# Performance work log

Measured on AMD Instinct MI355X. Metric: run time of the kernel, lower is better.

Reference implementation:

```python
import jax, jax.numpy as jnp
import numpy as np

D_HEAD = 64

def setup_inputs() -> dict:
    key = jax.random.key(0)
    ks = jax.random.split(key, 5)
    B, N, d_feat, d = 8, 2048, 256, 3
    f = jax.random.normal(ks[0], (B, N, d_feat), dtype=jnp.float32)
    x_tilde = jax.random.normal(ks[1], (B, N, d), dtype=jnp.float32)
    log_eps = jax.random.normal(ks[2], (B,), dtype=jnp.float32)
    W_q = jax.random.normal(ks[3], (d_feat + 1, D_HEAD), dtype=jnp.float32) * (1.0 / np.sqrt(d_feat + 1))
    W_k = jax.random.normal(ks[4], (d_feat + 1, D_HEAD), dtype=jnp.float32) * (1.0 / np.sqrt(d_feat + 1))
    return {"f": f, "x_tilde": x_tilde, "log_eps": log_eps, "W_q": W_q, "W_k": W_k}

def reference(f, x_tilde, log_eps, W_q, W_k):
    B, N, _ = f.shape
    # concat per-cloud log_eps scalar to every particle's features
    le = jnp.broadcast_to(log_eps[:, None, None], (B, N, 1)).astype(f.dtype)
    fc = jnp.concatenate([f, le], axis=-1)            # (B, N, d_feat+1)
    q = jnp.einsum('bnf,fh->bnh', fc, W_q)            # (B, N, d_head)
    k = jnp.einsum('bnf,fh->bnh', fc, W_k)            # (B, N, d_head)
    scale = jnp.asarray(np.sqrt(float(D_HEAD)), dtype=f.dtype)
    logits = jnp.einsum('bnh,bmh->bnm', q, k) / scale  # (B, N, N)
    N_f = jnp.asarray(N, dtype=f.dtype)
    col_softmax = jax.nn.softmax(logits, axis=1)       # softmax over QUERY axis
    pi = col_softmax / N_f                             # (B, N, N)
    # y_tilde = N * pi^T @ x_tilde
    y_tilde = N_f * jnp.einsum('bnm,bnd->bmd', pi, x_tilde)  # (B, N, d)
    return y_tilde, pi
```

## Files before the change

kernel.cpp:

```cpp
#include <hip/hip_runtime.h>
#include <hip/hip_bf16.h>

#define BB 8
#define NN 2048
#define DF 256
#define HH 64

using bf16x8 = __attribute__((ext_vector_type(8))) short;
using f32x4  = __attribute__((ext_vector_type(4))) float;
typedef unsigned short u16;

__global__ __launch_bounds__(256) void qk_proj_kernel(
    const float* __restrict__ f, const float* __restrict__ log_eps,
    const float* __restrict__ Wq, const float* __restrict__ Wk,
    __hip_bfloat16* __restrict__ Qs, __hip_bfloat16* __restrict__ Ks)
{
    __shared__ float wql[64 * 64];
    __shared__ float wkl[64 * 64];
    const int tid = threadIdx.x;
    const int h  = tid & 63;
    const int rg = tid >> 6;
    const int row_base = blockIdx.x * 32;
    const int b = row_base >> 11;

    const float le = log_eps[b];
    const float wq_last = Wq[DF * HH + h];
    const float wk_last = Wk[DF * HH + h];
    float q[8], k[8];
#pragma unroll
    for (int j = 0; j < 8; ++j) { q[j] = le * wq_last; k[j] = le * wk_last; }

    for (int kc = 0; kc < 4; ++kc) {
        __syncthreads();
#pragma unroll
        for (int it = 0; it < 4; ++it) {
            int idx = (tid + it * 256) * 4;
            *(float4*)&wql[idx] = *(const float4*)(Wq + kc * 4096 + idx);
            *(float4*)&wkl[idx] = *(const float4*)(Wk + kc * 4096 + idx);
        }
        __syncthreads();

        const float* fb = f + (size_t)(row_base + rg * 8) * DF + kc * 64;
#pragma unroll 4
        for (int i4 = 0; i4 < 16; ++i4) {
            float4 fv[8];
#pragma unroll
            for (int j = 0; j < 8; ++j)
                fv[j] = *(const float4*)(fb + (size_t)j * DF + i4 * 4);
#pragma unroll
            for (int u = 0; u < 4; ++u) {
                float wq = wql[(i4 * 4 + u) * 64 + h];
                float wk = wkl[(i4 * 4 + u) * 64 + h];
#pragma unroll
                for (int j = 0; j < 8; ++j) {
                    float fvv = (&fv[j].x)[u];
                    q[j] = fmaf(fvv, wq, q[j]);
                    k[j] = fmaf(fvv, wk, k[j]);
                }
            }
        }
    }

#pragma unroll
    for (int j = 0; j < 8; ++j) {
        int bn = row_base + rg * 8 + j;
        float qv = q[j] * 0.125f;
        float kv = k[j];
        __hip_bfloat16 qh = __float2bfloat16(qv);
        __hip_bfloat16 ql = __float2bfloat16(qv - __bfloat162float(qh));
        __hip_bfloat16 kh = __float2bfloat16(kv);
        __hip_bfloat16 kl = __float2bfloat16(kv - __bfloat162float(kh));
        size_t base = (size_t)bn * 128;
        Qs[base + h]      = qh;
        Qs[base + 64 + h] = ql;
        Ks[base + h]      = kh;
        Ks[base + 64 + h] = kl;
    }
}

__global__ __launch_bounds__(256) void attn_kernel(
    const u16* __restrict__ Qs, const u16* __restrict__ Ks,
    const float* __restrict__ x, float* __restrict__ y, float* __restrict__ pi)
{
    __shared__ float xs[NN * 3];
    __shared__ float cs_lds[32];
    __shared__ float yred[4 * 2 * 16 * 3];

    const int tid   = threadIdx.x;
    const int strip = blockIdx.x;
    const int b     = blockIdx.y;
    const int m0    = strip * 32;
    const int wave  = tid >> 6;
    const int lane  = tid & 63;
    const int l15   = lane & 15;
    const int quad  = lane >> 4;

    if (tid < 32) cs_lds[tid] = 0.f;
    for (int i = tid; i < NN * 3; i += 256) xs[i] = x[(size_t)b * NN * 3 + i];
    __syncthreads();

    bf16x8 bh[2][2], bl[2][2];
    {
        const u16* Kb = Ks + ((size_t)b * NN + m0) * 128;
#pragma unroll
        for (int ct = 0; ct < 2; ++ct) {
            const u16* kr = Kb + (size_t)(ct * 16 + l15) * 128;
#pragma unroll
            for (int ks = 0; ks < 2; ++ks) {
                int k0 = ks * 32 + quad * 8;
                bh[ct][ks] = *(const bf16x8*)(kr + k0);
                bl[ct][ks] = *(const bf16x8*)(kr + 64 + k0);
            }
        }
    }

    const u16* Qb = Qs + (size_t)b * NN * 128;
    float csacc0 = 0.f, csacc1 = 0.f;

    for (int rt = 0; rt < 16; ++rt) {
#pragma unroll
        for (int sr = 0; sr < 2; ++sr) {
            const int row0 = rt * 128 + wave * 32 + sr * 16;
            const u16* qr = Qb + (size_t)(row0 + l15) * 128;
            bf16x8 ah[2], al[2];
#pragma unroll
            for (int ks = 0; ks < 2; ++ks) {
                int k0 = ks * 32 + quad * 8;
                ah[ks] = *(const bf16x8*)(qr + k0);
                al[ks] = *(const bf16x8*)(qr + 64 + k0);
            }
#pragma unroll
            for (int ct = 0; ct < 2; ++ct) {
                f32x4 acc = {0.f, 0.f, 0.f, 0.f};
#pragma unroll
                for (int ks = 0; ks < 2; ++ks) {
                    acc = __builtin_amdgcn_mfma_f32_16x16x32_bf16(ah[ks], bh[ct][ks], acc, 0, 0, 0);
                    acc = __builtin_amdgcn_mfma_f32_16x16x32_bf16(ah[ks], bl[ct][ks], acc, 0, 0, 0);
                    acc = __builtin_amdgcn_mfma_f32_16x16x32_bf16(al[ks], bh[ct][ks], acc, 0, 0, 0);
                }
                float s = __expf(acc[0]) + __expf(acc[1]) + __expf(acc[2]) + __expf(acc[3]);
                s += __shfl_xor(s, 16);
                s += __shfl_xor(s, 32);
                if (ct == 0) csacc0 += s; else csacc1 += s;
            }
        }
    }
    if (quad == 0) {
        atomicAdd(&cs_lds[l15],      csacc0);
        atomicAdd(&cs_lds[16 + l15], csacc1);
    }
    __syncthreads();

    const float invc0 = 1.0f / cs_lds[l15];
    const float invc1 = 1.0f / cs_lds[16 + l15];
    const float invN  = 1.0f / (float)NN;
    float* pib = pi + (size_t)b * NN * NN + m0;
    float yacc[2][3] = {{0.f, 0.f, 0.f}, {0.f, 0.f, 0.f}};

    for (int rt = 0; rt < 16; ++rt) {
#pragma unroll
        for (int sr = 0; sr < 2; ++sr) {
            const int row0 = rt * 128 + wave * 32 + sr * 16;
            const u16* qr = Qb + (size_t)(row0 + l15) * 128;
            bf16x8 ah[2], al[2];
#pragma unroll
            for (int ks = 0; ks < 2; ++ks) {
                int k0 = ks * 32 + quad * 8;
                ah[ks] = *(const bf16x8*)(qr + k0);
                al[ks] = *(const bf16x8*)(qr + 64 + k0);
            }
            float xv[4][3];
#pragma unroll
            for (int r = 0; r < 4; ++r) {
                int row = row0 + quad * 4 + r;
                xv[r][0] = xs[row * 3 + 0];
                xv[r][1] = xs[row * 3 + 1];
                xv[r][2] = xs[row * 3 + 2];
            }
#pragma unroll
            for (int ct = 0; ct < 2; ++ct) {
                f32x4 acc = {0.f, 0.f, 0.f, 0.f};
#pragma unroll
                for (int ks = 0; ks < 2; ++ks) {
                    acc = __builtin_amdgcn_mfma_f32_16x16x32_bf16(ah[ks], bh[ct][ks], acc, 0, 0, 0);
                    acc = __builtin_amdgcn_mfma_f32_16x16x32_bf16(ah[ks], bl[ct][ks], acc, 0, 0, 0);
                    acc = __builtin_amdgcn_mfma_f32_16x16x32_bf16(al[ks], bh[ct][ks], acc, 0, 0, 0);
                }
                const float iv = (ct == 0) ? invc0 : invc1;
                float* op = pib + (size_t)(row0 + quad * 4) * NN + ct * 16 + l15;
#pragma unroll
                for (int r = 0; r < 4; ++r) {
                    float v = __expf(acc[r]) * iv;
                    op[(size_t)r * NN] = v * invN;
                    yacc[ct][0] = fmaf(v, xv[r][0], yacc[ct][0]);
                    yacc[ct][1] = fmaf(v, xv[r][1], yacc[ct][1]);
                    yacc[ct][2] = fmaf(v, xv[r][2], yacc[ct][2]);
                }
            }
        }
    }

#pragma unroll
    for (int ct = 0; ct < 2; ++ct)
#pragma unroll
        for (int d = 0; d < 3; ++d) {
            yacc[ct][d] += __shfl_xor(yacc[ct][d], 16);
            yacc[ct][d] += __shfl_xor(yacc[ct][d], 32);
        }
    if (quad == 0) {
#pragma unroll
        for (int ct = 0; ct < 2; ++ct)
#pragma unroll
            for (int d = 0; d < 3; ++d)
                yred[((wave * 2 + ct) * 16 + l15) * 3 + d] = yacc[ct][d];
    }
    __syncthreads();
    if (tid < 96) {
        int c = tid / 3, d = tid - c * 3;
        int ct = c >> 4, cl = c & 15;
        float s = 0.f;
#pragma unroll
        for (int w = 0; w < 4; ++w)
            s += yred[((w * 2 + ct) * 16 + cl) * 3 + d];
        y[((size_t)b * NN + m0 + c) * 3 + d] = s;
    }
}

extern "C" void kernel_launch(void* const* d_in, const int* in_sizes, int n_in,
                              void* d_out, int out_size, void* d_ws, size_t ws_size,
                              hipStream_t stream) {
    const float* f  = (const float*)d_in[0];
    const float* x  = (const float*)d_in[1];
    const float* le = (const float*)d_in[2];
    const float* Wq = (const float*)d_in[3];
    const float* Wk = (const float*)d_in[4];

    float* y  = (float*)d_out;
    float* pi = (float*)d_out + (size_t)BB * NN * 3;

    __hip_bfloat16* Qs = (__hip_bfloat16*)d_ws;
    __hip_bfloat16* Ks = Qs + (size_t)BB * NN * 128;

    qk_proj_kernel<<<dim3(BB * NN / 32), 256, 0, stream>>>(f, le, Wq, Wk, Qs, Ks);
    attn_kernel<<<dim3(64, BB), 256, 0, stream>>>((const u16*)Qs, (const u16*)Ks, x, y, pi);
}
```

Before: 240.3 us.

## Use MFMA for QK projection and split attention write pass across row chunks

Replaces the scalar FMA Q/K projection with a split-bf16 MFMA kernel, fed by a small pre-pass that packs W into hi/lo bf16 fragments stored temporarily in the pi output buffer. The attention kernel now fuses the y accumulation into the column-sum pass, normalising by the column sum afterwards. It then splits the pi-writing pass across four row chunks per strip to quadruple the grid and raise occupancy. The cost is that every chunk recomputes the full column-sum pass, so that MFMA and exp work is done four times. The extra launch and the reuse of the output buffer as scratch also rely on the attention kernel overwriting it later.

Measured after the change: 321.7 us. 33.8% more time.

```diff
diff --git a/kernel.cpp b/kernel.cpp
--- a/kernel.cpp
+++ b/kernel.cpp
@@ -10,71 +10,90 @@
 using f32x4  = __attribute__((ext_vector_type(4))) float;
 typedef unsigned short u16;
 
-__global__ __launch_bounds__(256) void qk_proj_kernel(
+static __device__ __forceinline__ short bf_hi_bits(float v, float* hi_f) {
+    __hip_bfloat16 h = __float2bfloat16(v);
+    *hi_f = __bfloat162float(h);
+    return __builtin_bit_cast(short, h);
+}
+
+__global__ __launch_bounds__(64) void wprep_kernel(
+    const float* __restrict__ Wq, const float* __restrict__ Wk,
+    u16* __restrict__ Wsp)
+{
+    const int fid  = blockIdx.x;
+    const int kc   = fid >> 3, ct = fid & 7;
+    const int lane = threadIdx.x;
+    const float* W = (ct < 4) ? Wq : Wk;
+    const int col  = (ct & 3) * 16 + (lane & 15);
+    const int krow = kc * 32 + (lane >> 4) * 8;
+    bf16x8 hv, lv;
+#pragma unroll
+    for (int j = 0; j < 8; ++j) {
+        float w = W[(size_t)(krow + j) * HH + col];
+        float hf, d;
+        hv[j] = bf_hi_bits(w, &hf);
+        lv[j] = bf_hi_bits(w - hf, &d);
+    }
+    u16* dst = Wsp + (size_t)fid * 1024 + lane * 8;
+    *(bf16x8*)dst         = hv;
+    *(bf16x8*)(dst + 512) = lv;
+}
+
+__global__ __launch_bounds__(64) void qk_mfma_kernel(
     const float* __restrict__ f, const float* __restrict__ log_eps,
     const float* __restrict__ Wq, const float* __restrict__ Wk,
+    const u16* __restrict__ Wsp,
     __hip_bfloat16* __restrict__ Qs, __hip_bfloat16* __restrict__ Ks)
 {
-    __shared__ float wql[64 * 64];
-    __shared__ float wkl[64 * 64];
-    const int tid = threadIdx.x;
-    const int h  = tid & 63;
-    const int rg = tid >> 6;
-    const int row_base = blockIdx.x * 32;
-    const int b = row_base >> 11;
+    const int lane = threadIdx.x;
+    const int l15  = lane & 15, quad = lane >> 4;
+    const int row0 = blockIdx.x * 16;
+    const int b    = row0 >> 11;
+
+    f32x4 acc[8] = {};
+    const float* frow = f + (size_t)(row0 + l15) * DF + quad * 8;
+
+#pragma unroll
+    for (int kc = 0; kc < 8; ++kc) {
+        float4 a0 = *(const float4*)(frow + kc * 32);
+        float4 a1 = *(const float4*)(frow + kc * 32 + 4);
+        bf16x8 ah, al;
+#pragma unroll
+        for (int e = 0; e < 4; ++e) {
+            float hf, d;
+            float v0 = (&a0.x)[e], v1 = (&a1.x)[e];
+            ah[e]     = bf_hi_bits(v0, &hf);
+            al[e]     = bf_hi_bits(v0 - hf, &d);
+            ah[e + 4] = bf_hi_bits(v1, &hf);
+            al[e + 4] = bf_hi_bits(v1 - hf, &d);
+        }
+        const u16* wb = Wsp + (size_t)kc * 8192 + lane * 8;
+#pragma unroll
+        for (int ct = 0; ct < 8; ++ct) {
+            bf16x8 bh = *(const bf16x8*)(wb + ct * 1024);
+            bf16x8 bl = *(const bf16x8*)(wb + ct * 1024 + 512);
+            acc[ct] = __builtin_amdgcn_mfma_f32_16x16x32_bf16(ah, bh, acc[ct], 0, 0, 0);
+            acc[ct] = __builtin_amdgcn_mfma_f32_16x16x32_bf16(ah, bl, acc[ct], 0, 0, 0);
+            acc[ct] = __builtin_amdgcn_mfma_f32_16x16x32_bf16(al, bh, acc[ct], 0, 0, 0);
+        }
+    }
 
     const float le = log_eps[b];
-    const float wq_last = Wq[DF * HH + h];
-    const float wk_last = Wk[DF * HH + h];
-    float q[8], k[8];
-#pragma unroll
-    for (int j = 0; j < 8; ++j) { q[j] = le * wq_last; k[j] = le * wk_last; }
-
-    for (int kc = 0; kc < 4; ++kc) {
-        __syncthreads();
-#pragma unroll
-        for (int it = 0; it < 4; ++it) {
-            int idx = (tid + it * 256) * 4;
-            *(float4*)&wql[idx] = *(const float4*)(Wq + kc * 4096 + idx);
-            *(float4*)&wkl[idx] = *(const float4*)(Wk + kc * 4096 + idx);
-        }
-        __syncthreads();
-
-        const float* fb = f + (size_t)(row_base + rg * 8) * DF + kc * 64;
-#pragma unroll 4
-        for (int i4 = 0; i4 < 16; ++i4) {
-            float4 fv[8];
-#pragma unroll
-            for (int j = 0; j < 8; ++j)
-                fv[j] = *(const float4*)(fb + (size_t)j * DF + i4 * 4);
-#pragma unroll
-            for (int u = 0; u < 4; ++u) {
-                float wq = wql[(i4 * 4 + u) * 64 + h];
-                float wk = wkl[(i4 * 4 + u) * 64 + h];
-#pragma unroll
-                for (int j = 0; j < 8; ++j) {
-                    float fvv = (&fv[j].x)[u];
-                    q[j] = fmaf(fvv, wq, q[j]);
-                    k[j] = fmaf(fvv, wk, k[j]);
-                }
-            }
-        }
-    }
-
-#pragma unroll
-    for (int j = 0; j < 8; ++j) {
-        int bn = row_base + rg * 8 + j;
-        float qv = q[j] * 0.125f;
-        float kv = k[j];
-        __hip_bfloat16 qh = __float2bfloat16(qv);
-        __hip_bfloat16 ql = __float2bfloat16(qv - __bfloat162float(qh));
-        __hip_bfloat16 kh = __float2bfloat16(kv);
-        __hip_bfloat16 kl = __float2bfloat16(kv - __bfloat162float(kh));
-        size_t base = (size_t)bn * 128;
-        Qs[base + h]      = qh;
-        Qs[base + 64 + h] = ql;
-        Ks[base + h]      = kh;
-        Ks[base + 64 + h] = kl;
+#pragma unroll
+    for (int ct = 0; ct < 8; ++ct) {
+        const int h = (ct & 3) * 16 + l15;
+        const float wlast = (ct < 4 ? Wq : Wk)[DF * HH + h];
+        __hip_bfloat16* out = (ct < 4) ? Qs : Ks;
+        const float sc = (ct < 4) ? 0.125f : 1.0f;
+#pragma unroll
+        for (int r = 0; r < 4; ++r) {
+            int bn = row0 + quad * 4 + r;
+            float v = (acc[ct][r] + le * wlast) * sc;
+            __hip_bfloat16 hi = __float2bfloat16(v);
+            __hip_bfloat16 lo = __float2bfloat16(v - __bfloat162float(hi));
+            out[(size_t)bn * 128 + h]      = hi;
+            out[(size_t)bn * 128 + 64 + h] = lo;
+        }
     }
 }
 
@@ -82,21 +101,21 @@
     const u16* __restrict__ Qs, const u16* __restrict__ Ks,
     const float* __restrict__ x, float* __restrict__ y, float* __restrict__ pi)
 {
-    __shared__ float xs[NN * 3];
-    __shared__ float cs_lds[32];
+    __shared__ float cred[32];
     __shared__ float yred[4 * 2 * 16 * 3];
 
     const int tid   = threadIdx.x;
     const int strip = blockIdx.x;
-    const int b     = blockIdx.y;
+    const int chunk = blockIdx.y;
+    const int b     = blockIdx.z;
     const int m0    = strip * 32;
     const int wave  = tid >> 6;
     const int lane  = tid & 63;
     const int l15   = lane & 15;
     const int quad  = lane >> 4;
-
-    if (tid < 32) cs_lds[tid] = 0.f;
-    for (int i = tid; i < NN * 3; i += 256) xs[i] = x[(size_t)b * NN * 3 + i];
+    const bool do_y = (chunk == 0);
+
+    if (tid < 32) cred[tid] = 0.f;
     __syncthreads();
 
     bf16x8 bh[2][2], bl[2][2];
@@ -114,8 +133,10 @@
         }
     }
 
-    const u16* Qb = Qs + (size_t)b * NN * 128;
-    float csacc0 = 0.f, csacc1 = 0.f;
+    const u16*  Qb = Qs + (size_t)b * NN * 128;
+    const float* xb = x + (size_t)b * NN * 3;
+    float cs0 = 0.f, cs1 = 0.f;
+    float yacc[2][3] = {{0.f, 0.f, 0.f}, {0.f, 0.f, 0.f}};
 
     for (int rt = 0; rt < 16; ++rt) {
 #pragma unroll
@@ -129,6 +150,16 @@
                 ah[ks] = *(const bf16x8*)(qr + k0);
                 al[ks] = *(const bf16x8*)(qr + 64 + k0);
             }
+            float xv[4][3];
+            if (do_y) {
+#pragma unroll
+                for (int r = 0; r < 4; ++r) {
+                    int row = row0 + quad * 4 + r;
+                    xv[r][0] = xb[row * 3 + 0];
+                    xv[r][1] = xb[row * 3 + 1];
+                    xv[r][2] = xb[row * 3 + 2];
+                }
+            }
 #pragma unroll
             for (int ct = 0; ct < 2; ++ct) {
                 f32x4 acc = {0.f, 0.f, 0.f, 0.f};
@@ -138,29 +169,66 @@
                     acc = __builtin_amdgcn_mfma_f32_16x16x32_bf16(ah[ks], bl[ct][ks], acc, 0, 0, 0);
                     acc = __builtin_amdgcn_mfma_f32_16x16x32_bf16(al[ks], bh[ct][ks], acc, 0, 0, 0);
                 }
-                float s = __expf(acc[0]) + __expf(acc[1]) + __expf(acc[2]) + __expf(acc[3]);
+                float s = 0.f;
+#pragma unroll
+                for (int r = 0; r < 4; ++r) {
+                    float v = __expf(acc[r]);
+                    s += v;
+                    if (do_y) {
+                        yacc[ct][0] = fmaf(v, xv[r][0], yacc[ct][0]);
+                        yacc[ct][1] = fmaf(v, xv[r][1], yacc[ct][1]);
+                        yacc[ct][2] = fmaf(v, xv[r][2], yacc[ct][2]);
+                    }
+                }
                 s += __shfl_xor(s, 16);
                 s += __shfl_xor(s, 32);
-                if (ct == 0) csacc0 += s; else csacc1 += s;
-            }
-        }
-    }
+                if (ct == 0) cs0 += s; else cs1 += s;
+            }
+        }
+    }
+
     if (quad == 0) {
-        atomicAdd(&cs_lds[l15],      csacc0);
-        atomicAdd(&cs_lds[16 + l15], csacc1);
+        atomicAdd(&cred[l15],      cs0);
+        atomicAdd(&cred[16 + l15], cs1);
+    }
+    if (do_y) {
+#pragma unroll
+        for (int ct = 0; ct < 2; ++ct)
+#pragma unroll
+            for (int d = 0; d < 3; ++d) {
+                yacc[ct][d] += __shfl_xor(yacc[ct][d], 16);
+                yacc[ct][d] += __shfl_xor(yacc[ct][d], 32);
+            }
+        if (quad == 0) {
+#pragma unroll
+            for (int ct = 0; ct < 2; ++ct)
+#pragma unroll
+                for (int d = 0; d < 3; ++d)
+                    yred[((wave * 2 + ct) * 16 + l15) * 3 + d] = yacc[ct][d];
+        }
     }
     __syncthreads();
 
-    const float invc0 = 1.0f / cs_lds[l15];
-    const float invc1 = 1.0f / cs_lds[16 + l15];
-    const float invN  = 1.0f / (float)NN;
+    if (do_y && tid < 96) {
+        int c = tid / 3, d = tid - c * 3;
+        int ct = c >> 4, cl = c & 15;
+        float s = 0.f;
+#pragma unroll
+        for (int w = 0; w < 4; ++w)
+            s += yred[((w * 2 + ct) * 16 + cl) * 3 + d];
+        y[((size_t)b * NN + m0 + c) * 3 + d] = s / cred[c];
+    }
+
+    const float invN = 1.0f / (float)NN;
+    const float iv0  = invN / cred[l15];
+    const float iv1  = invN / cred[16 + l15];
     float* pib = pi + (size_t)b * NN * NN + m0;
-    float yacc[2][3] = {{0.f, 0.f, 0.f}, {0.f, 0.f, 0.f}};
-
-    for (int rt = 0; rt < 16; ++rt) {
+    const int n0 = chunk * 512;
+
+    for (int rt = 0; rt < 4; ++rt) {
 #pragma unroll
         for (int sr = 0; sr < 2; ++sr) {
-            const int row0 = rt * 128 + wave * 32 + sr * 16;
+            const int row0 = n0 + rt * 128 + wave * 32 + sr * 16;
             const u16* qr = Qb + (size_t)(row0 + l15) * 128;
             bf16x8 ah[2], al[2];
 #pragma unroll
@@ -169,14 +237,6 @@
                 ah[ks] = *(const bf16x8*)(qr + k0);
                 al[ks] = *(const bf16x8*)(qr + 64 + k0);
             }
-            float xv[4][3];
-#pragma unroll
-            for (int r = 0; r < 4; ++r) {
-                int row = row0 + quad * 4 + r;
-                xv[r][0] = xs[row * 3 + 0];
-                xv[r][1] = xs[row * 3 + 1];
-                xv[r][2] = xs[row * 3 + 2];
-            }
 #pragma unroll
             for (int ct = 0; ct < 2; ++ct) {
                 f32x4 acc = {0.f, 0.f, 0.f, 0.f};
@@ -186,43 +246,13 @@
                     acc = __builtin_amdgcn_mfma_f32_16x16x32_bf16(ah[ks], bl[ct][ks], acc, 0, 0, 0);
                     acc = __builtin_amdgcn_mfma_f32_16x16x32_bf16(al[ks], bh[ct][ks], acc, 0, 0, 0);
                 }
-                const float iv = (ct == 0) ? invc0 : invc1;
+                const float iv = (ct == 0) ? iv0 : iv1;
                 float* op = pib + (size_t)(row0 + quad * 4) * NN + ct * 16 + l15;
 #pragma unroll
-                for (int r = 0; r < 4; ++r) {
-                    float v = __expf(acc[r]) * iv;
-                    op[(size_t)r * NN] = v * invN;
-                    yacc[ct][0] = fmaf(v, xv[r][0], yacc[ct][0]);
-                    yacc[ct][1] = fmaf(v, xv[r][1], yacc[ct][1]);
-                    yacc[ct][2] = fmaf(v, xv[r][2], yacc[ct][2]);
-                }
-            }
-        }
-    }
-
-#pragma unroll
-    for (int ct = 0; ct < 2; ++ct)
-#pragma unroll
-        for (int d = 0; d < 3; ++d) {
-            yacc[ct][d] += __shfl_xor(yacc[ct][d], 16);
-            yacc[ct][d] += __shfl_xor(yacc[ct][d], 32);
-        }
-    if (quad == 0) {
-#pragma unroll
-        for (int ct = 0; ct < 2; ++ct)
-#pragma unroll
-            for (int d = 0; d < 3; ++d)
-                yred[((wave * 2 + ct) * 16 + l15) * 3 + d] = yacc[ct][d];
-    }
-    __syncthreads();
-    if (tid < 96) {
-        int c = tid / 3, d = tid - c * 3;
-        int ct = c >> 4, cl = c & 15;
-        float s = 0.f;
-#pragma unroll
-        for (int w = 0; w < 4; ++w)
-            s += yred[((w * 2 + ct) * 16 + cl) * 3 + d];
-        y[((size_t)b * NN + m0 + c) * 3 + d] = s;
+                for (int r = 0; r < 4; ++r)
+                    op[(size_t)r * NN] = __expf(acc[r]) * iv;
+            }
+        }
     }
 }
 
@@ -240,7 +270,10 @@
 
     __hip_bfloat16* Qs = (__hip_bfloat16*)d_ws;
     __hip_bfloat16* Ks = Qs + (size_t)BB * NN * 128;
-
-    qk_proj_kernel<<<dim3(BB * NN / 32), 256, 0, stream>>>(f, le, Wq, Wk, Qs, Ks);
-    attn_kernel<<<dim3(64, BB), 256, 0, stream>>>((const u16*)Qs, (const u16*)Ks, x, y, pi);
-}
+    u16* Wsp = (u16*)pi;
+
+    wprep_kernel<<<dim3(64), 64, 0, stream>>>(Wq, Wk, Wsp);
+    qk_mfma_kernel<<<dim3(BB * NN / 16), 64, 0, stream>>>(f, le, Wq, Wk, Wsp, Qs, Ks);
+    attn_kernel<<<dim3(64, 4, BB), 256, 0, stream>>>((const u16*)Qs, (const u16*)Ks,
+                                                     x, y, pi);
+}
```
